# Kernel tuning notes

Hardware: AMD Instinct MI355X
Metric: run time of the kernel (lower is better)

The kernel has to match this reference:

```python
import jax, jax.numpy as jnp
import numpy as np

F_DIM = 1024
D = F_DIM // 2          # trunk width (divisor=2)
T = 1024                # contextlen
B = 32
PI = 256
VF = 256
N_HEADS = 4
EPS = 1e-5


def _posenc(seq_len, d):
    pos = jnp.arange(seq_len, dtype=jnp.float32)[:, None]
    div = jnp.exp(jnp.arange(0, d, 2, dtype=jnp.float32) * (-np.log(10000.0) / d))
    pe = jnp.zeros((seq_len, d), dtype=jnp.float32)
    pe = pe.at[:, 0::2].set(jnp.sin(pos * div))
    pe = pe.at[:, 1::2].set(jnp.cos(pos * div))
    return pe


def _ln(x, g, b):
    mu = x.mean(-1, keepdims=True)
    var = ((x - mu) ** 2).mean(-1, keepdims=True)
    return (x - mu) / jnp.sqrt(var + EPS) * g + b


def setup_inputs() -> dict:
    key = jax.random.key(0)
    ks = iter(jax.random.split(key, 40))
    w = lambda shape: jax.random.normal(next(ks), shape, dtype=jnp.float32) * 0.02
    inp = {
        "features": jax.random.normal(next(ks), (B, T, F_DIM), dtype=jnp.float32),
        "enc_w1": w((F_DIM, D)), "enc_b1": jnp.zeros((D,), jnp.float32),
        "enc_w2": w((D, D)),     "enc_b2": jnp.zeros((D,), jnp.float32),
        "qkv_w": w((D, 3 * D)),  "qkv_b": jnp.zeros((3 * D,), jnp.float32),
        "lam": jnp.float32(0.8),
        "out_w": w((D, D)),      "out_b": jnp.zeros((D,), jnp.float32),
        "ln1_g": jnp.ones((D,), jnp.float32), "ln1_b": jnp.zeros((D,), jnp.float32),
        "ffn_w1": w((D, F_DIM)), "ffn_b1": jnp.zeros((F_DIM,), jnp.float32),
        "ffn_w2": w((F_DIM, D)), "ffn_b2": jnp.zeros((D,), jnp.float32),
        "ln2_g": jnp.ones((D,), jnp.float32), "ln2_b": jnp.zeros((D,), jnp.float32),
        "act_w1": w((D, F_DIM)),       "act_b1": jnp.zeros((F_DIM,), jnp.float32),
        "act_w2": w((F_DIM, 2 * F_DIM)), "act_b2": jnp.zeros((2 * F_DIM,), jnp.float32),
        "act_w3": w((2 * F_DIM, PI)),  "act_b3": jnp.zeros((PI,), jnp.float32),
        "cr_w1": w((D, F_DIM)),        "cr_b1": jnp.zeros((F_DIM,), jnp.float32),
        "cr_w2": w((F_DIM, 2 * F_DIM)), "cr_b2": jnp.zeros((2 * F_DIM,), jnp.float32),
        "cr_w3": w((2 * F_DIM, VF)),   "cr_b3": jnp.zeros((VF,), jnp.float32),
    }
    return inp


def reference(features, enc_w1, enc_b1, enc_w2, enc_b2, qkv_w, qkv_b, lam,
              out_w, out_b, ln1_g, ln1_b, ffn_w1, ffn_b1, ffn_w2, ffn_b2,
              ln2_g, ln2_b, act_w1, act_b1, act_w2, act_b2, act_w3, act_b3,
              cr_w1, cr_b1, cr_w2, cr_b2, cr_w3, cr_b3):
    b, t, f = features.shape
    # encoder MLP: feature_dim -> d -> d with ReLU
    y = jax.nn.relu(features @ enc_w1 + enc_b1)
    y = jax.nn.relu(y @ enc_w2 + enc_b2)            # (B,T,D)
    d = y.shape[-1]
    y = y + _posenc(t, d)
    # differential dual-softmax attention (no head split; head_dim only scales)
    qkv = y @ qkv_w + qkv_b
    q, k, v = jnp.split(qkv, 3, axis=-1)
    q1, q2 = jnp.split(q, 2, axis=-1)
    k1, k2 = jnp.split(k, 2, axis=-1)
    scale = 1.0 / np.sqrt(d // N_HEADS)
    a1 = jax.nn.softmax(jnp.einsum('btc,bsc->bts', q1, k1) * scale, axis=-1)
    a2 = jax.nn.softmax(jnp.einsum('btc,bsc->bts', q2, k2) * scale, axis=-1)
    diff = a1 - lam * a2
    attn = jnp.einsum('bts,bsd->btd', diff, v)      # (B,T,D)
    # faithful to torch: transpose(0,1).contiguous().view(B,-1,D)
    attn = jnp.swapaxes(attn, 0, 1).reshape(b, t, d)
    attn = attn @ out_w + out_b
    y = _ln(y + attn, ln1_g, ln1_b)
    z = jax.nn.relu(y @ ffn_w1 + ffn_b1) @ ffn_w2 + ffn_b2
    y = _ln(y + z, ln2_g, ln2_b)                     # (B,T,D)
    # actor / critic heads, then take last timestep
    a = jax.nn.relu(y @ act_w1 + act_b1)
    a = jax.nn.relu(a @ act_w2 + act_b2)
    a = a @ act_w3 + act_b3
    c = jax.nn.relu(y @ cr_w1 + cr_b1)
    c = jax.nn.relu(c @ cr_w2 + cr_b2)
    c = c @ cr_w3 + cr_b3
    return (a[:, -1, :], c[:, -1, :])
```

## Files before the change

kernel.cpp:

```cpp
#include <hip/hip_runtime.h>
#include <hip/hip_bf16.h>
#include <math.h>

#define TDIM 1024
#define FDIM 1024
#define DDIM 512

typedef __attribute__((ext_vector_type(8))) short bf16x8;
typedef __attribute__((ext_vector_type(4))) float f32x4;

__device__ __forceinline__ float posenc_val(int t, int c) {
    int j = c >> 1;
    float dv = expf(-9.210340371976184f * (float)(2 * j) * (1.0f / 512.0f));
    float arg = (float)t * dv;
    return (c & 1) ? cosf(arg) : sinf(arg);
}

__device__ __forceinline__ ushort f2bf(float f) {
    __hip_bfloat16 h = __float2bfloat16(f);
    return *reinterpret_cast<ushort*>(&h);
}

__global__ __launch_bounds__(256)
void conv_bf16(const float* __restrict__ src, ushort* __restrict__ dst, int n4)
{
    int i = blockIdx.x * 256 + threadIdx.x;
    if (i < n4) {
        float4 v = ((const float4*)src)[i];
        ushort4 o;
        o.x = f2bf(v.x); o.y = f2bf(v.y); o.z = f2bf(v.z); o.w = f2bf(v.w);
        ((ushort4*)dst)[i] = o;
    }
}

__global__ __launch_bounds__(256)
void convT_bf16(const float* __restrict__ W, int ldw, int col0,
                ushort* __restrict__ Wt, int K)
{
    __shared__ float t[32][33];
    const int k0 = blockIdx.y * 32, n0 = blockIdx.x * 32;
    const int x = threadIdx.x & 31, y = threadIdx.x >> 5;
    #pragma unroll
    for (int yy = y; yy < 32; yy += 8)
        t[yy][x] = W[(size_t)(k0 + yy) * ldw + col0 + n0 + x];
    __syncthreads();
    #pragma unroll
    for (int yy = y; yy < 32; yy += 8)
        Wt[(size_t)(n0 + yy) * K + k0 + x] = f2bf(t[x][yy]);
}

__global__ __launch_bounds__(256)
void mfma_gemm(const ushort* __restrict__ A, const ushort* __restrict__ Bt,
               const float* __restrict__ bias,
               float* __restrict__ C, int ldc,
               ushort* __restrict__ Cbf, int ldcb,
               int K, int relu, int addpe)
{
    __shared__ __align__(16) ushort Al[64 * 64];
    __shared__ __align__(16) ushort Bl[64 * 64];
    const int tid = threadIdx.x;
    const int m0 = blockIdx.y * 64;
    const int n0 = blockIdx.x * 64;
    const int lane = tid & 63;
    const int wv = tid >> 6;
    const int wr = wv >> 1, wc = wv & 1;
    const int fr = lane & 15, g = lane >> 4;

    f32x4 acc[2][2] = {};

    const int r0 = tid >> 3;
    const int c0 = tid & 7;

    for (int k0 = 0; k0 < K; k0 += 64) {
        #pragma unroll
        for (int it = 0; it < 2; ++it) {
            int r = r0 + it * 32;
            uint4 va = *(const uint4*)(A + (size_t)(m0 + r) * K + k0 + c0 * 8);
            *(uint4*)((char*)Al + r * 128 + ((c0 ^ (r & 7)) << 4)) = va;
            uint4 vb = *(const uint4*)(Bt + (size_t)(n0 + r) * K + k0 + c0 * 8);
            *(uint4*)((char*)Bl + r * 128 + ((c0 ^ (r & 7)) << 4)) = vb;
        }
        __syncthreads();
        #pragma unroll
        for (int h = 0; h < 2; ++h) {
            bf16x8 af[2], bff[2];
            #pragma unroll
            for (int i = 0; i < 2; ++i) {
                int row = wr * 32 + i * 16 + fr;
                af[i] = *(const bf16x8*)((const char*)Al + row * 128 + (((h * 4 + g) ^ (row & 7)) << 4));
                int col = wc * 32 + i * 16 + fr;
                bff[i] = *(const bf16x8*)((const char*)Bl + col * 128 + (((h * 4 + g) ^ (col & 7)) << 4));
            }
            #pragma unroll
            for (int i = 0; i < 2; ++i)
                #pragma unroll
                for (int j = 0; j < 2; ++j)
                    acc[i][j] = __builtin_amdgcn_mfma_f32_16x16x32_bf16(af[i], bff[j], acc[i][j], 0, 0, 0);
        }
        __syncthreads();
    }

    #pragma unroll
    for (int j = 0; j < 2; ++j) {
        int n = n0 + wc * 32 + j * 16 + fr;
        float bv = bias ? bias[n] : 0.f;
        #pragma unroll
        for (int i = 0; i < 2; ++i) {
            #pragma unroll
            for (int q = 0; q < 4; ++q) {
                int m = m0 + wr * 32 + i * 16 + g * 4 + q;
                float v = acc[i][j][q] + bv;
                if (relu) v = fmaxf(v, 0.f);
                if (addpe) v += posenc_val(m, n);
                if (C)   C[(size_t)m * ldc + n] = v;
                if (Cbf) Cbf[(size_t)m * ldcb + n] = f2bf(v);
            }
        }
    }
}

template<int BK>
__global__ __launch_bounds__(256)
void gemm32d(const float* __restrict__ X0, const float* __restrict__ X1, long lda,
             const float* __restrict__ W0, const float* __restrict__ W1, long ldb,
             float* __restrict__ P, int N)
{
    __shared__ float Xs[32][BK + 4];
    __shared__ float Ws[BK][64];
    const float* A = blockIdx.z ? X1 : X0;
    const float* B = blockIdx.z ? W1 : W0;
    const int tid = threadIdx.x;
    const int n0 = blockIdx.x * 64;
    const int k0 = blockIdx.y * BK;

    {
        const int m  = tid >> 3;
        const int ks = (tid & 7) * (BK / 8);
        const float* src = A + (size_t)m * lda + k0 + ks;
        #pragma unroll
        for (int j = 0; j < BK / 32; ++j) {
            float4 v = *(const float4*)(src + j * 4);
            *(float4*)&Xs[m][ks + j * 4] = v;
        }
    }
    #pragma unroll
    for (int it = 0; it < BK / 16; ++it) {
        int e4  = it * 256 + tid;
        int row = e4 >> 4;
        int c4  = e4 & 15;
        float4 v = *(const float4*)(B + (size_t)(k0 + row) * ldb + n0 + c4 * 4);
        *(float4*)&Ws[row][c4 * 4] = v;
    }
    __syncthreads();

    const int tx = tid & 31;
    const int ty = tid >> 5;
    float acc[4][2] = {};
    #pragma unroll 8
    for (int k = 0; k < BK; k += 4) {
        float4 xv[4];
        #pragma unroll
        for (int i = 0; i < 4; ++i) xv[i] = *(const float4*)&Xs[ty * 4 + i][k];
        #pragma unroll
        for (int j = 0; j < 4; ++j) {
            float2 w = *(const float2*)&Ws[k + j][tx * 2];
            #pragma unroll
            for (int i = 0; i < 4; ++i) {
                float x = ((const float*)&xv[i])[j];
                acc[i][0] = fmaf(x, w.x, acc[i][0]);
                acc[i][1] = fmaf(x, w.y, acc[i][1]);
            }
        }
    }

    float* dst = P + (size_t)(blockIdx.z * gridDim.y + blockIdx.y) * 32 * N;
    #pragma unroll
    for (int i = 0; i < 4; ++i) {
        float2 v = make_float2(acc[i][0], acc[i][1]);
        *(float2*)(dst + (size_t)(ty * 4 + i) * N + n0 + tx * 2) = v;
    }
}

__global__ __launch_bounds__(256)
void finalized(const float* __restrict__ P, int KC, int N,
               const float* __restrict__ b0, const float* __restrict__ b1,
               float* __restrict__ Y0, float* __restrict__ Y1, int ldy,
               int do_relu, int perow)
{
    const int z = blockIdx.z;
    const float* bias = z ? b1 : b0;
    float* Y = z ? Y1 : Y0;
    const float* Pz = P + (size_t)z * KC * 32 * N;
    const int n = blockIdx.x * 256 + threadIdx.x;
    const int m = blockIdx.y;
    float s = bias ? bias[n] : 0.f;
    for (int kc = 0; kc < KC; ++kc) s += Pz[(size_t)(kc * 32 + m) * N + n];
    if (do_relu) s = fmaxf(s, 0.f);
    if (perow >= 0) s += posenc_val(perow, n);
    Y[(size_t)m * ldy + n] = s;
}

__global__ __launch_bounds__(256)
void scores_kernel(const float* __restrict__ KV, const float* __restrict__ Q32,
                   float* __restrict__ Psc)
{
    __shared__ float Kt[64][132];
    __shared__ float Qt[32][133];
    const int tid = threadIdx.x;
    const int s0 = blockIdx.x * 64;
    const int k0 = blockIdx.y * 128;

    #pragma unroll
    for (int it = 0; it < 8; ++it) {
        int e4 = it * 256 + tid;
        int r  = e4 >> 5;
        int c4 = e4 & 31;
        float4 v = *(const float4*)(KV + (size_t)(s0 + r) * 1024 + k0 + c4 * 4);
        *(float4*)&Kt[r][c4 * 4] = v;
    }
    #pragma unroll
    for (int it = 0; it < 4; ++it) {
        int e4 = it * 256 + tid;
        int r  = e4 >> 5;
        int c4 = e4 & 31;
        float4 v = *(const float4*)(Q32 + (size_t)r * 512 + k0 + c4 * 4);
        Qt[r][c4 * 4 + 0] = v.x;
        Qt[r][c4 * 4 + 1] = v.y;
        Qt[r][c4 * 4 + 2] = v.z;
        Qt[r][c4 * 4 + 3] = v.w;
    }
    __syncthreads();

    const int i  = tid & 31;
    const int sg = tid >> 5;
    float acc[8] = {};
    for (int k = 0; k < 128; ++k) {
        float q = Qt[i][k];
        #pragma unroll
        for (int j = 0; j < 8; ++j)
            acc[j] = fmaf(Kt[sg * 8 + j][k], q, acc[j]);
    }
    float* dst = Psc + (size_t)blockIdx.y * 1024 * 32;
    #pragma unroll
    for (int j = 0; j < 8; ++j)
        dst[(size_t)(s0 + sg * 8 + j) * 32 + i] = acc[j];
}

__global__ __launch_bounds__(256)
void softmax_diff(const float* __restrict__ Psc, const float* __restrict__ lam_p,
                  float* __restrict__ D)
{
    __shared__ float sc1[TDIM];
    __shared__ float sc2[TDIM];
    __shared__ float red[256];
    const int i = blockIdx.x;
    const int tid = threadIdx.x;
    const float scale = 0.08838834764831845f;
    for (int s = tid; s < TDIM; s += 256) {
        float a = Psc[(size_t)(0 * 1024 + s) * 32 + i] + Psc[(size_t)(1 * 1024 + s) * 32 + i];
        float b = Psc[(size_t)(2 * 1024 + s) * 32 + i] + Psc[(size_t)(3 * 1024 + s) * 32 + i];
        sc1[s] = a * scale;
        sc2[s] = b * scale;
    }
    __syncthreads();
    float m1 = -INFINITY, m2 = -INFINITY;
    for (int s = tid; s < TDIM; s += 256) { m1 = fmaxf(m1, sc1[s]); m2 = fmaxf(m2, sc2[s]); }
    red[tid] = m1; __syncthreads();
    for (int o = 128; o > 0; o >>= 1) { if (tid < o) red[tid] = fmaxf(red[tid], red[tid + o]); __syncthreads(); }
    m1 = red[0]; __syncthreads();
    red[tid] = m2; __syncthreads();
    for (int o = 128; o > 0; o >>= 1) { if (tid < o) red[tid] = fmaxf(red[tid], red[tid + o]); __syncthreads(); }
    m2 = red[0]; __syncthreads();
    float t1 = 0.f, t2 = 0.f;
    for (int s = tid; s < TDIM; s += 256) { t1 += expf(sc1[s] - m1); t2 += expf(sc2[s] - m2); }
    red[tid] = t1; __syncthreads();
    for (int o = 128; o > 0; o >>= 1) { if (tid < o) red[tid] += red[tid + o]; __syncthreads(); }
    t1 = red[0]; __syncthreads();
    red[tid] = t2; __syncthreads();
    for (int o = 128; o > 0; o >>= 1) { if (tid < o) red[tid] += red[tid + o]; __syncthreads(); }
    t2 = red[0]; __syncthreads();
    const float inv1 = 1.f / t1, inv2 = 1.f / t2;
    const float lam = *lam_p;
    for (int s = tid; s < TDIM; s += 256)
        D[(size_t)i * TDIM + s] = expf(sc1[s] - m1) * inv1 - lam * expf(sc2[s] - m2) * inv2;
}

__global__ __launch_bounds__(256)
void ln_kernel(const float* __restrict__ X, const float* __restrict__ R,
               const float* __restrict__ g, const float* __restrict__ b,
               float* __restrict__ Y)
{
    __shared__ float red[256];
    const int m = blockIdx.x;
    const int tid = threadIdx.x;
    float v0 = X[m * DDIM + tid]       + R[m * DDIM + tid];
    float v1 = X[m * DDIM + 256 + tid] + R[m * DDIM + 256 + tid];
    red[tid] = v0 + v1; __syncthreads();
    for (int o = 128; o > 0; o >>= 1) { if (tid < o) red[tid] += red[tid + o]; __syncthreads(); }
    const float mu = red[0] * (1.0f / 512.0f);
    __syncthreads();
    float d0 = v0 - mu, d1 = v1 - mu;
    red[tid] = d0 * d0 + d1 * d1; __syncthreads();
    for (int o = 128; o > 0; o >>= 1) { if (tid < o) red[tid] += red[tid + o]; __syncthreads(); }
    const float var = red[0] * (1.0f / 512.0f);
    const float inv = 1.0f / sqrtf(var + 1e-5f);
    Y[m * DDIM + tid]       = d0 * inv * g[tid]       + b[tid];
    Y[m * DDIM + 256 + tid] = d1 * inv * g[256 + tid] + b[256 + tid];
}

static void smallM2(const float* A0, const float* A1, long lda,
                    const float* B0, const float* B1, long ldb,
                    const float* b0, const float* b1,
                    float* Y0, float* Y1, int ldy, int K, int N,
                    int relu, int perow, float* P, int nz, hipStream_t stream)
{
    const int BK = (K == 1024 && N == 2048) ? 128 : 64;
    const int KC = K / BK;
    dim3 blk(256);
    if (BK == 128)
        gemm32d<128><<<dim3(N / 64, KC, nz), blk, 0, stream>>>(A0, A1, lda, B0, B1, ldb, P, N);
    else
        gemm32d<64><<<dim3(N / 64, KC, nz), blk, 0, stream>>>(A0, A1, lda, B0, B1, ldb, P, N);
    finalized<<<dim3(N / 256, 32, nz), blk, 0, stream>>>(P, KC, N, b0, b1, Y0, Y1, ldy, relu, perow);
}

extern "C" void kernel_launch(void* const* d_in, const int* in_sizes, int n_in,
                              void* d_out, int out_size, void* d_ws, size_t ws_size,
                              hipStream_t stream)
{
    const float* features = (const float*)d_in[0];
    const float* enc_w1 = (const float*)d_in[1];
    const float* enc_b1 = (const float*)d_in[2];
    const float* enc_w2 = (const float*)d_in[3];
    const float* enc_b2 = (const float*)d_in[4];
    const float* qkv_w  = (const float*)d_in[5];
    const float* qkv_b  = (const float*)d_in[6];
    const float* lam    = (const float*)d_in[7];
    const float* out_w  = (const float*)d_in[8];
    const float* out_b  = (const float*)d_in[9];
    const float* ln1_g  = (const float*)d_in[10];
    const float* ln1_b  = (const float*)d_in[11];
    const float* ffn_w1 = (const float*)d_in[12];
    const float* ffn_b1 = (const float*)d_in[13];
    const float* ffn_w2 = (const float*)d_in[14];
    const float* ffn_b2 = (const float*)d_in[15];
    const float* ln2_g  = (const float*)d_in[16];
    const float* ln2_b  = (const float*)d_in[17];
    const float* act_w1 = (const float*)d_in[18];
    const float* act_b1 = (const float*)d_in[19];
    const float* act_w2 = (const float*)d_in[20];
    const float* act_b2 = (const float*)d_in[21];
    const float* act_w3 = (const float*)d_in[22];
    const float* act_b3 = (const float*)d_in[23];
    const float* cr_w1  = (const float*)d_in[24];
    const float* cr_b1  = (const float*)d_in[25];
    const float* cr_w2  = (const float*)d_in[26];
    const float* cr_b2  = (const float*)d_in[27];
    const float* cr_w3  = (const float*)d_in[28];
    const float* cr_b3  = (const float*)d_in[29];
    float* out = (float*)d_out;

    char* base = (char*)d_ws;
    ushort* feat_bf = (ushort*)(base + 0);
    ushort* w1T     = (ushort*)(base + (2u << 20));
    ushort* w2T     = (ushort*)(base + (3u << 20));
    ushort* kvwT    = (ushort*)(base + 3670016);
    float*  Ppart   = (float*)(base + 0);
    ushort* H1bf    = (ushort*)(base + 4718592);
    float*  Y31     = (float*)(base + 5767168);
    ushort* Y31bf   = (ushort*)(base + 7864320);
    float*  KV      = (float*)(base + 8912896);
    float*  Psc     = (float*)(base + 13107200);
    float*  Dbuf    = (float*)(base + 13631488);
    float*  h32     = (float*)(base + 13762560);
    float*  ylast   = h32    + 32 * 512;
    float*  Q32     = ylast  + 32 * 512;
    float*  attn32  = Q32    + 32 * 512;
    float*  attnp   = attn32 + 32 * 512;
    float*  y1      = attnp  + 32 * 512;
    float*  y2      = y1     + 32 * 512;
    float*  zbuf    = y2     + 32 * 512;
    float*  hbufA   = zbuf   + 32 * 512;
    float*  hbufC   = hbufA  + 32 * 1024;
    float*  hbuf2A  = hbufC  + 32 * 1024;
    float*  hbuf2C  = hbuf2A + 32 * 2048;

    dim3 blk(256);

    conv_bf16<<<1024, blk, 0, stream>>>(features + (size_t)31 * TDIM * FDIM, feat_bf, 262144);
    convT_bf16<<<dim3(16, 32), blk, 0, stream>>>(enc_w1, DDIM, 0, w1T, FDIM);
    convT_bf16<<<dim3(16, 16), blk, 0, stream>>>(enc_w2, DDIM, 0, w2T, DDIM);
    convT_bf16<<<dim3(32, 16), blk, 0, stream>>>(qkv_w, 1536, 512, kvwT, DDIM);

    mfma_gemm<<<dim3(8, 16), blk, 0, stream>>>(feat_bf, w1T, enc_b1,
                                               (float*)nullptr, 0, H1bf, DDIM, FDIM, 1, 0);
    mfma_gemm<<<dim3(8, 16), blk, 0, stream>>>(H1bf, w2T, enc_b2,
                                               Y31, DDIM, Y31bf, DDIM, DDIM, 1, 1);
    mfma_gemm<<<dim3(16, 16), blk, 0, stream>>>(Y31bf, kvwT, qkv_b + 512,
                                                KV, 1024, (ushort*)nullptr, 0, DDIM, 0, 0);

    smallM2(features + (size_t)(TDIM - 1) * FDIM, nullptr, (long)TDIM * FDIM,
            enc_w1, nullptr, DDIM, enc_b1, nullptr, h32, nullptr, DDIM,
            FDIM, DDIM, 1, -1, Ppart, 1, stream);
    smallM2(h32, nullptr, DDIM, enc_w2, nullptr, DDIM, enc_b2, nullptr,
            ylast, nullptr, DDIM, DDIM, DDIM, 1, TDIM - 1, Ppart, 1, stream);
    smallM2(Y31 + 31 * DDIM, nullptr, 32 * DDIM, qkv_w, nullptr, 1536, qkv_b, nullptr,
            Q32, nullptr, DDIM, DDIM, DDIM, 0, -1, Ppart, 1, stream);

    scores_kernel<<<dim3(16, 4), blk, 0, stream>>>(KV, Q32, Psc);
    softmax_diff<<<32, blk, 0, stream>>>(Psc, lam, Dbuf);
    gemm32d<64><<<dim3(8, 16, 1), blk, 0, stream>>>(Dbuf, nullptr, 1024, KV + 512, nullptr, 1024, Ppart, 512);
    finalized<<<dim3(2, 32, 1), blk, 0, stream>>>(Ppart, 16, 512, nullptr, nullptr, attn32, nullptr, 512, 0, -1);

    smallM2(attn32, nullptr, DDIM, out_w, nullptr, DDIM, out_b, nullptr,
            attnp, nullptr, DDIM, DDIM, DDIM, 0, -1, Ppart, 1, stream);
    ln_kernel<<<32, blk, 0, stream>>>(ylast, attnp, ln1_g, ln1_b, y1);
    smallM2(y1, nullptr, DDIM, ffn_w1, nullptr, FDIM, ffn_b1, nullptr,
            hbufA, nullptr, FDIM, DDIM, FDIM, 1, -1, Ppart, 1, stream);
    smallM2(hbufA, nullptr, FDIM, ffn_w2, nullptr, DDIM, ffn_b2, nullptr,
            zbuf, nullptr, DDIM, FDIM, DDIM, 0, -1, Ppart, 1, stream);
    ln_kernel<<<32, blk, 0, stream>>>(y1, zbuf, ln2_g, ln2_b, y2);

    smallM2(y2, y2, DDIM, act_w1, cr_w1, FDIM, act_b1, cr_b1,
            hbufA, hbufC, FDIM, DDIM, FDIM, 1, -1, Ppart, 2, stream);
    smallM2(hbufA, hbufC, FDIM, act_w2, cr_w2, 2 * FDIM, act_b2, cr_b2,
            hbuf2A, hbuf2C, 2 * FDIM, FDIM, 2 * FDIM, 1, -1, Ppart, 2, stream);
    smallM2(hbuf2A, hbuf2C, 2 * FDIM, act_w3, cr_w3, 256, act_b3, cr_b3,
            out, out + 8192, 256, 2 * FDIM, 256, 0, -1, Ppart, 2, stream);
}
```

Measured before the change: 175.6 us.

## Fuse small kernels, merge split-K reductions into consumers, cut launch count

Merges the weight transposes and the first last-row GEMM into one prep kernel, and fuses the fp32-to-bf16 feature conversion into the MFMA GEMM's A load. Several independent stages are co-scheduled in shared launches. Split-K finalize kernels are removed by having the next GEMM or LayerNorm sum the partial buffers with bias and relu on load. The full QKV projection is computed in one MFMA GEMM, so the separate Q GEMM goes away. This cuts launch count and intermediate round trips, at the cost of redundant partial-sum reads inside each consumer block.

```diff
diff --git a/kernel.cpp b/kernel.cpp
--- a/kernel.cpp
+++ b/kernel.cpp
@@ -7,6 +7,7 @@
 #define DDIM 512
 
 typedef __attribute__((ext_vector_type(8))) short bf16x8;
+typedef __attribute__((ext_vector_type(8))) ushort u16x8;
 typedef __attribute__((ext_vector_type(4))) float f32x4;
 
 __device__ __forceinline__ float posenc_val(int t, int c) {
@@ -21,24 +22,102 @@
     return *reinterpret_cast<ushort*>(&h);
 }
 
-__global__ __launch_bounds__(256)
-void conv_bf16(const float* __restrict__ src, ushort* __restrict__ dst, int n4)
-{
-    int i = blockIdx.x * 256 + threadIdx.x;
-    if (i < n4) {
-        float4 v = ((const float4*)src)[i];
-        ushort4 o;
-        o.x = f2bf(v.x); o.y = f2bf(v.y); o.z = f2bf(v.z); o.w = f2bf(v.w);
-        ((ushort4*)dst)[i] = o;
-    }
-}
-
-__global__ __launch_bounds__(256)
-void convT_bf16(const float* __restrict__ W, int ldw, int col0,
-                ushort* __restrict__ Wt, int K)
-{
-    __shared__ float t[32][33];
-    const int k0 = blockIdx.y * 32, n0 = blockIdx.x * 32;
+template<int BK>
+__device__ __forceinline__ void g32_body(
+    const float* X, long lda,
+    const float* Pin, int KCx, const float* xbias, int xrelu,
+    const float* W, long ldb,
+    float* Pout, int N, int K,
+    int bx, int by, float* lds)
+{
+    float (*Xs)[BK + 4] = (float (*)[BK + 4])lds;
+    float (*Ws)[64]     = (float (*)[64])(lds + 32 * (BK + 4));
+    const int tid = threadIdx.x;
+    const int n0 = bx * 64, k0 = by * BK;
+
+    {
+        const int m  = tid >> 3;
+        const int ks = (tid & 7) * (BK / 8);
+        if (Pin) {
+            #pragma unroll
+            for (int j = 0; j < BK / 32; ++j) {
+                float4 a = make_float4(0.f, 0.f, 0.f, 0.f);
+                for (int c = 0; c < KCx; ++c) {
+                    float4 v = *(const float4*)(Pin + (size_t)(c * 32 + m) * K + k0 + ks + j * 4);
+                    a.x += v.x; a.y += v.y; a.z += v.z; a.w += v.w;
+                }
+                if (xbias) {
+                    float4 bv = *(const float4*)(xbias + k0 + ks + j * 4);
+                    a.x += bv.x; a.y += bv.y; a.z += bv.z; a.w += bv.w;
+                }
+                if (xrelu) {
+                    a.x = fmaxf(a.x, 0.f); a.y = fmaxf(a.y, 0.f);
+                    a.z = fmaxf(a.z, 0.f); a.w = fmaxf(a.w, 0.f);
+                }
+                *(float4*)&Xs[m][ks + j * 4] = a;
+            }
+        } else {
+            const float* src = X + (size_t)m * lda + k0 + ks;
+            #pragma unroll
+            for (int j = 0; j < BK / 32; ++j)
+                *(float4*)&Xs[m][ks + j * 4] = *(const float4*)(src + j * 4);
+        }
+    }
+    #pragma unroll
+    for (int it = 0; it < BK / 16; ++it) {
+        int e4  = it * 256 + tid;
+        int row = e4 >> 4;
+        int c4  = e4 & 15;
+        *(float4*)&Ws[row][c4 * 4] = *(const float4*)(W + (size_t)(k0 + row) * ldb + n0 + c4 * 4);
+    }
+    __syncthreads();
+
+    const int tx = tid & 31;
+    const int ty = tid >> 5;
+    float acc[4][2] = {};
+    #pragma unroll 8
+    for (int k = 0; k < BK; k += 4) {
+        float4 xv[4];
+        #pragma unroll
+        for (int i = 0; i < 4; ++i) xv[i] = *(const float4*)&Xs[ty * 4 + i][k];
+        #pragma unroll
+        for (int j = 0; j < 4; ++j) {
+            float2 w = *(const float2*)&Ws[k + j][tx * 2];
+            #pragma unroll
+            for (int i = 0; i < 4; ++i) {
+                float x = ((const float*)&xv[i])[j];
+                acc[i][0] = fmaf(x, w.x, acc[i][0]);
+                acc[i][1] = fmaf(x, w.y, acc[i][1]);
+            }
+        }
+    }
+    float* dst = Pout + (size_t)by * 32 * N;
+    #pragma unroll
+    for (int i = 0; i < 4; ++i)
+        *(float2*)(dst + (size_t)(ty * 4 + i) * N + n0 + tx * 2) = make_float2(acc[i][0], acc[i][1]);
+}
+
+template<int BK>
+__global__ __launch_bounds__(256) void g32k(
+    const float* X0, const float* X1, long lda,
+    const float* Pin0, const float* Pin1, int KCx,
+    const float* xb0, const float* xb1, int xrelu,
+    const float* W0, const float* W1, long ldb,
+    float* Pout, int N, int K)
+{
+    __shared__ __align__(16) float lds[32 * (BK + 4) + BK * 64];
+    const int z = blockIdx.z;
+    g32_body<BK>(z ? X1 : X0, lda, z ? Pin1 : Pin0, KCx, z ? xb1 : xb0, xrelu,
+                 z ? W1 : W0, ldb,
+                 Pout + (size_t)z * gridDim.y * 32 * N,
+                 N, K, blockIdx.x, blockIdx.y, lds);
+}
+
+__device__ __forceinline__ void convT_body(const float* W, int ldw, int col0,
+                                           ushort* Wt, int K, int bx, int by, float* lds)
+{
+    float (*t)[33] = (float (*)[33])lds;
+    const int k0 = by * 32, n0 = bx * 32;
     const int x = threadIdx.x & 31, y = threadIdx.x >> 5;
     #pragma unroll
     for (int yy = y; yy < 32; yy += 8)
@@ -49,18 +128,18 @@
         Wt[(size_t)(n0 + yy) * K + k0 + x] = f2bf(t[x][yy]);
 }
 
-__global__ __launch_bounds__(256)
-void mfma_gemm(const ushort* __restrict__ A, const ushort* __restrict__ Bt,
-               const float* __restrict__ bias,
-               float* __restrict__ C, int ldc,
-               ushort* __restrict__ Cbf, int ldcb,
-               int K, int relu, int addpe)
-{
-    __shared__ __align__(16) ushort Al[64 * 64];
-    __shared__ __align__(16) ushort Bl[64 * 64];
+__device__ __forceinline__ void mfma_body(
+    const void* Aptr, int af32, long lda,
+    const ushort* Bt, const float* bias,
+    float* C, int ldc, ushort* Cbf, int ldcb,
+    int K, int relu, int addpe,
+    int bx, int by, char* smem)
+{
+    ushort* Al = (ushort*)smem;
+    ushort* Bl = Al + 64 * 64;
     const int tid = threadIdx.x;
-    const int m0 = blockIdx.y * 64;
-    const int n0 = blockIdx.x * 64;
+    const int m0 = by * 64;
+    const int n0 = bx * 64;
     const int lane = tid & 63;
     const int wv = tid >> 6;
     const int wr = wv >> 1, wc = wv & 1;
@@ -75,8 +154,20 @@
         #pragma unroll
         for (int it = 0; it < 2; ++it) {
             int r = r0 + it * 32;
-            uint4 va = *(const uint4*)(A + (size_t)(m0 + r) * K + k0 + c0 * 8);
-            *(uint4*)((char*)Al + r * 128 + ((c0 ^ (r & 7)) << 4)) = va;
+            if (af32) {
+                const float* Af = (const float*)Aptr;
+                const float* s = Af + (size_t)(m0 + r) * lda + k0 + c0 * 8;
+                float4 u = *(const float4*)s;
+                float4 v = *(const float4*)(s + 4);
+                u16x8 pv;
+                pv[0] = f2bf(u.x); pv[1] = f2bf(u.y); pv[2] = f2bf(u.z); pv[3] = f2bf(u.w);
+                pv[4] = f2bf(v.x); pv[5] = f2bf(v.y); pv[6] = f2bf(v.z); pv[7] = f2bf(v.w);
+                *(u16x8*)((char*)Al + r * 128 + ((c0 ^ (r & 7)) << 4)) = pv;
+            } else {
+                const ushort* Au = (const ushort*)Aptr;
+                uint4 va = *(const uint4*)(Au + (size_t)(m0 + r) * lda + k0 + c0 * 8);
+                *(uint4*)((char*)Al + r * 128 + ((c0 ^ (r & 7)) << 4)) = va;
+            }
             uint4 vb = *(const uint4*)(Bt + (size_t)(n0 + r) * K + k0 + c0 * 8);
             *(uint4*)((char*)Bl + r * 128 + ((c0 ^ (r & 7)) << 4)) = vb;
         }
@@ -119,103 +210,67 @@
     }
 }
 
-template<int BK>
-__global__ __launch_bounds__(256)
-void gemm32d(const float* __restrict__ X0, const float* __restrict__ X1, long lda,
-             const float* __restrict__ W0, const float* __restrict__ W1, long ldb,
-             float* __restrict__ P, int N)
-{
-    __shared__ float Xs[32][BK + 4];
-    __shared__ float Ws[BK][64];
-    const float* A = blockIdx.z ? X1 : X0;
-    const float* B = blockIdx.z ? W1 : W0;
+__global__ __launch_bounds__(256) void mfma_k(
+    const void* A, int af32, long lda, const ushort* Bt, const float* bias,
+    float* C, int ldc, ushort* Cbf, int ldcb, int K, int relu, int pe)
+{
+    __shared__ __align__(16) char smem[16384];
+    mfma_body(A, af32, lda, Bt, bias, C, ldc, Cbf, ldcb, K, relu, pe,
+              blockIdx.x, blockIdx.y, smem);
+}
+
+__global__ __launch_bounds__(256) void prep_k(
+    const float* features, const float* enc_w1, const float* qkv_w, const float* enc_w2,
+    ushort* w1T, ushort* w2T, ushort* qkvT, float* P_enc1)
+{
+    __shared__ __align__(16) float lds[6272];
+    int t = blockIdx.x;
+    if (t < 128) {
+        g32_body<64>(features + (size_t)1023 * FDIM, (long)TDIM * FDIM,
+                     nullptr, 0, nullptr, 0,
+                     enc_w1, DDIM, P_enc1, 512, 1024, t & 7, t >> 3, lds);
+    } else if (t < 640) {
+        int u = t - 128;
+        convT_body(enc_w1, 512, 0, w1T, 1024, u & 15, u >> 4, lds);
+    } else if (t < 896) {
+        int u = t - 640;
+        convT_body(enc_w2, 512, 0, w2T, 512, u & 15, u >> 4, lds);
+    } else {
+        int u = t - 896;
+        convT_body(qkv_w, 1536, 0, qkvT, 512, u % 48, u / 48, lds);
+    }
+}
+
+__global__ __launch_bounds__(256) void stage2_k(
+    const float* features31, const ushort* w1T, const float* enc_b1, ushort* H1bf,
+    const float* P_enc1, const float* enc_w2, float* P_enc2)
+{
+    __shared__ __align__(16) char smem[25600];
+    int t = blockIdx.x;
+    if (t < 128) {
+        mfma_body(features31, 1, 1024, w1T, enc_b1, nullptr, 0, H1bf, 512,
+                  1024, 1, 0, t & 7, t >> 3, smem);
+    } else {
+        int u = t - 128;
+        g32_body<64>(nullptr, 0, P_enc1, 16, enc_b1, 1,
+                     enc_w2, 512, P_enc2, 512, 512, u & 7, u >> 3, (float*)smem);
+    }
+}
+
+__device__ void scores_body(const float* QKV, float* Psc, int bxs, int byc, char* smem)
+{
+    float (*Kt)[132] = (float (*)[132])smem;
+    float (*Qt)[133] = (float (*)[133])(smem + 64 * 132 * 4);
     const int tid = threadIdx.x;
-    const int n0 = blockIdx.x * 64;
-    const int k0 = blockIdx.y * BK;
-
-    {
-        const int m  = tid >> 3;
-        const int ks = (tid & 7) * (BK / 8);
-        const float* src = A + (size_t)m * lda + k0 + ks;
-        #pragma unroll
-        for (int j = 0; j < BK / 32; ++j) {
-            float4 v = *(const float4*)(src + j * 4);
-            *(float4*)&Xs[m][ks + j * 4] = v;
-        }
-    }
-    #pragma unroll
-    for (int it = 0; it < BK / 16; ++it) {
-        int e4  = it * 256 + tid;
-        int row = e4 >> 4;
-        int c4  = e4 & 15;
-        float4 v = *(const float4*)(B + (size_t)(k0 + row) * ldb + n0 + c4 * 4);
-        *(float4*)&Ws[row][c4 * 4] = v;
-    }
-    __syncthreads();
-
-    const int tx = tid & 31;
-    const int ty = tid >> 5;
-    float acc[4][2] = {};
-    #pragma unroll 8
-    for (int k = 0; k < BK; k += 4) {
-        float4 xv[4];
-        #pragma unroll
-        for (int i = 0; i < 4; ++i) xv[i] = *(const float4*)&Xs[ty * 4 + i][k];
-        #pragma unroll
-        for (int j = 0; j < 4; ++j) {
-            float2 w = *(const float2*)&Ws[k + j][tx * 2];
-            #pragma unroll
-            for (int i = 0; i < 4; ++i) {
-                float x = ((const float*)&xv[i])[j];
-                acc[i][0] = fmaf(x, w.x, acc[i][0]);
-                acc[i][1] = fmaf(x, w.y, acc[i][1]);
-            }
-        }
-    }
-
-    float* dst = P + (size_t)(blockIdx.z * gridDim.y + blockIdx.y) * 32 * N;
-    #pragma unroll
-    for (int i = 0; i < 4; ++i) {
-        float2 v = make_float2(acc[i][0], acc[i][1]);
-        *(float2*)(dst + (size_t)(ty * 4 + i) * N + n0 + tx * 2) = v;
-    }
-}
-
-__global__ __launch_bounds__(256)
-void finalized(const float* __restrict__ P, int KC, int N,
-               const float* __restrict__ b0, const float* __restrict__ b1,
-               float* __restrict__ Y0, float* __restrict__ Y1, int ldy,
-               int do_relu, int perow)
-{
-    const int z = blockIdx.z;
-    const float* bias = z ? b1 : b0;
-    float* Y = z ? Y1 : Y0;
-    const float* Pz = P + (size_t)z * KC * 32 * N;
-    const int n = blockIdx.x * 256 + threadIdx.x;
-    const int m = blockIdx.y;
-    float s = bias ? bias[n] : 0.f;
-    for (int kc = 0; kc < KC; ++kc) s += Pz[(size_t)(kc * 32 + m) * N + n];
-    if (do_relu) s = fmaxf(s, 0.f);
-    if (perow >= 0) s += posenc_val(perow, n);
-    Y[(size_t)m * ldy + n] = s;
-}
-
-__global__ __launch_bounds__(256)
-void scores_kernel(const float* __restrict__ KV, const float* __restrict__ Q32,
-                   float* __restrict__ Psc)
-{
-    __shared__ float Kt[64][132];
-    __shared__ float Qt[32][133];
-    const int tid = threadIdx.x;
-    const int s0 = blockIdx.x * 64;
-    const int k0 = blockIdx.y * 128;
+    const int s0 = bxs * 64;
+    const int k0 = byc * 128;
 
     #pragma unroll
     for (int it = 0; it < 8; ++it) {
         int e4 = it * 256 + tid;
         int r  = e4 >> 5;
         int c4 = e4 & 31;
-        float4 v = *(const float4*)(KV + (size_t)(s0 + r) * 1024 + k0 + c4 * 4);
+        float4 v = *(const float4*)(QKV + (size_t)(s0 + r) * 1536 + 512 + k0 + c4 * 4);
         *(float4*)&Kt[r][c4 * 4] = v;
     }
     #pragma unroll
@@ -223,7 +278,7 @@
         int e4 = it * 256 + tid;
         int r  = e4 >> 5;
         int c4 = e4 & 31;
-        float4 v = *(const float4*)(Q32 + (size_t)r * 512 + k0 + c4 * 4);
+        float4 v = *(const float4*)(QKV + (size_t)(32 * r + 31) * 1536 + k0 + c4 * 4);
         Qt[r][c4 * 4 + 0] = v.x;
         Qt[r][c4 * 4 + 1] = v.y;
         Qt[r][c4 * 4 + 2] = v.z;
@@ -240,15 +295,35 @@
         for (int j = 0; j < 8; ++j)
             acc[j] = fmaf(Kt[sg * 8 + j][k], q, acc[j]);
     }
-    float* dst = Psc + (size_t)blockIdx.y * 1024 * 32;
+    float* dst = Psc + (size_t)byc * 1024 * 32;
     #pragma unroll
     for (int j = 0; j < 8; ++j)
         dst[(size_t)(s0 + sg * 8 + j) * 32 + i] = acc[j];
 }
 
-__global__ __launch_bounds__(256)
-void softmax_diff(const float* __restrict__ Psc, const float* __restrict__ lam_p,
-                  float* __restrict__ D)
+__global__ __launch_bounds__(256) void stage5_k(
+    const float* QKV, float* Psc,
+    const float* P_enc2, const float* enc_b2, float* ylast)
+{
+    __shared__ __align__(16) char smem[50816];
+    int t = blockIdx.x;
+    if (t < 64) {
+        scores_body(QKV, Psc, t & 15, t >> 4, smem);
+    } else {
+        int blk = t - 64;
+        for (int idx = threadIdx.x; idx < 4 * 512; idx += 256) {
+            int r = idx >> 9, c = idx & 511;
+            int m = blk * 4 + r;
+            float s = enc_b2[c];
+            for (int cc = 0; cc < 8; ++cc) s += P_enc2[(size_t)(cc * 32 + m) * 512 + c];
+            s = fmaxf(s, 0.f) + posenc_val(1023, c);
+            ylast[m * 512 + c] = s;
+        }
+    }
+}
+
+__global__ __launch_bounds__(256) void softmax_diff(
+    const float* __restrict__ Psc, const float* __restrict__ lam_p, float* __restrict__ D)
 {
     __shared__ float sc1[TDIM];
     __shared__ float sc2[TDIM];
@@ -285,16 +360,22 @@
         D[(size_t)i * TDIM + s] = expf(sc1[s] - m1) * inv1 - lam * expf(sc2[s] - m2) * inv2;
 }
 
-__global__ __launch_bounds__(256)
-void ln_kernel(const float* __restrict__ X, const float* __restrict__ R,
-               const float* __restrict__ g, const float* __restrict__ b,
-               float* __restrict__ Y)
+__global__ __launch_bounds__(256) void ln_red(
+    const float* __restrict__ Pin, int KC, const float* __restrict__ bias,
+    const float* __restrict__ R, const float* __restrict__ g, const float* __restrict__ b,
+    float* __restrict__ Y)
 {
     __shared__ float red[256];
     const int m = blockIdx.x;
     const int tid = threadIdx.x;
-    float v0 = X[m * DDIM + tid]       + R[m * DDIM + tid];
-    float v1 = X[m * DDIM + 256 + tid] + R[m * DDIM + 256 + tid];
+    float v0 = bias ? bias[tid] : 0.f;
+    float v1 = bias ? bias[tid + 256] : 0.f;
+    for (int c = 0; c < KC; ++c) {
+        v0 += Pin[(size_t)(c * 32 + m) * 512 + tid];
+        v1 += Pin[(size_t)(c * 32 + m) * 512 + tid + 256];
+    }
+    v0 += R[m * 512 + tid];
+    v1 += R[m * 512 + tid + 256];
     red[tid] = v0 + v1; __syncthreads();
     for (int o = 128; o > 0; o >>= 1) { if (tid < o) red[tid] += red[tid + o]; __syncthreads(); }
     const float mu = red[0] * (1.0f / 512.0f);
@@ -304,24 +385,22 @@
     for (int o = 128; o > 0; o >>= 1) { if (tid < o) red[tid] += red[tid + o]; __syncthreads(); }
     const float var = red[0] * (1.0f / 512.0f);
     const float inv = 1.0f / sqrtf(var + 1e-5f);
-    Y[m * DDIM + tid]       = d0 * inv * g[tid]       + b[tid];
-    Y[m * DDIM + 256 + tid] = d1 * inv * g[256 + tid] + b[256 + tid];
-}
-
-static void smallM2(const float* A0, const float* A1, long lda,
-                    const float* B0, const float* B1, long ldb,
-                    const float* b0, const float* b1,
-                    float* Y0, float* Y1, int ldy, int K, int N,
-                    int relu, int perow, float* P, int nz, hipStream_t stream)
-{
-    const int BK = (K == 1024 && N == 2048) ? 128 : 64;
-    const int KC = K / BK;
-    dim3 blk(256);
-    if (BK == 128)
-        gemm32d<128><<<dim3(N / 64, KC, nz), blk, 0, stream>>>(A0, A1, lda, B0, B1, ldb, P, N);
-    else
-        gemm32d<64><<<dim3(N / 64, KC, nz), blk, 0, stream>>>(A0, A1, lda, B0, B1, ldb, P, N);
-    finalized<<<dim3(N / 256, 32, nz), blk, 0, stream>>>(P, KC, N, b0, b1, Y0, Y1, ldy, relu, perow);
+    Y[m * 512 + tid]       = d0 * inv * g[tid]       + b[tid];
+    Y[m * 512 + 256 + tid] = d1 * inv * g[256 + tid] + b[256 + tid];
+}
+
+__global__ __launch_bounds__(256) void fin_out(
+    const float* __restrict__ P, const float* __restrict__ b0, const float* __restrict__ b1,
+    float* __restrict__ out)
+{
+    const int m = blockIdx.x;
+    const int z = blockIdx.y;
+    const int n = threadIdx.x;
+    const float* bias = z ? b1 : b0;
+    const float* Pz = P + (size_t)z * 16 * 32 * 256;
+    float s = bias[n];
+    for (int c = 0; c < 16; ++c) s += Pz[(size_t)(c * 32 + m) * 256 + n];
+    out[z * 8192 + m * 256 + n] = s;
 }
 
 extern "C" void kernel_launch(void* const* d_in, const int* in_sizes, int n_in,
@@ -361,70 +440,56 @@
     float* out = (float*)d_out;
 
     char* base = (char*)d_ws;
-    ushort* feat_bf = (ushort*)(base + 0);
-    ushort* w1T     = (ushort*)(base + (2u << 20));
-    ushort* w2T     = (ushort*)(base + (3u << 20));
-    ushort* kvwT    = (ushort*)(base + 3670016);
-    float*  Ppart   = (float*)(base + 0);
-    ushort* H1bf    = (ushort*)(base + 4718592);
-    float*  Y31     = (float*)(base + 5767168);
-    ushort* Y31bf   = (ushort*)(base + 7864320);
-    float*  KV      = (float*)(base + 8912896);
-    float*  Psc     = (float*)(base + 13107200);
-    float*  Dbuf    = (float*)(base + 13631488);
-    float*  h32     = (float*)(base + 13762560);
-    float*  ylast   = h32    + 32 * 512;
-    float*  Q32     = ylast  + 32 * 512;
-    float*  attn32  = Q32    + 32 * 512;
-    float*  attnp   = attn32 + 32 * 512;
-    float*  y1      = attnp  + 32 * 512;
-    float*  y2      = y1     + 32 * 512;
-    float*  zbuf    = y2     + 32 * 512;
-    float*  hbufA   = zbuf   + 32 * 512;
-    float*  hbufC   = hbufA  + 32 * 1024;
-    float*  hbuf2A  = hbufC  + 32 * 1024;
-    float*  hbuf2C  = hbuf2A + 32 * 2048;
-
+    ushort* w1T    = (ushort*)(base + 0x000000);
+    ushort* w2T    = (ushort*)(base + 0x100000);
+    ushort* qkvT   = (ushort*)(base + 0x180000);
+    ushort* H1bf   = (ushort*)(base + 0x300000);
+    ushort* Y31bf  = (ushort*)(base + 0x400000);
+    float*  QKV    = (float*)(base + 0x500000);
+    float*  Psc    = (float*)(base + 0xB00000);
+    float*  Dbuf   = (float*)(base + 0xB80000);
+    float*  ylast  = (float*)(base + 0xBA0000);
+    float*  y1     = (float*)(base + 0xBB0000);
+    float*  y2     = (float*)(base + 0xBC0000);
+    float*  P_enc1 = (float*)(base + 0xC00000);
+    float*  P_enc2 = (float*)(base + 0xD00000);
+    float*  P_attn = (float*)(base + 0xD80000);
+    float*  P_atp  = (float*)(base + 0xE80000);
+    float*  P_h    = (float*)(base + 0xF00000);
+    float*  P_z    = (float*)(base + 0x1000000);
+    float*  P_a1   = (float*)(base + 0x1100000);
+    float*  P_a2   = (float*)(base + 0x1300000);
+    float*  P_a3   = (float*)(base + 0x1700000);
+
+    const float* features31 = features + (size_t)31 * TDIM * FDIM;
     dim3 blk(256);
-
-    conv_bf16<<<1024, blk, 0, stream>>>(features + (size_t)31 * TDIM * FDIM, feat_bf, 262144);
-    convT_bf16<<<dim3(16, 32), blk, 0, stream>>>(enc_w1, DDIM, 0, w1T, FDIM);
-    convT_bf16<<<dim3(16, 16), blk, 0, stream>>>(enc_w2, DDIM, 0, w2T, DDIM);
-    convT_bf16<<<dim3(32, 16), blk, 0, stream>>>(qkv_w, 1536, 512, kvwT, DDIM);
-
-    mfma_gemm<<<dim3(8, 16), blk, 0, stream>>>(feat_bf, w1T, enc_b1,
-                                               (float*)nullptr, 0, H1bf, DDIM, FDIM, 1, 0);
-    mfma_gemm<<<dim3(8, 16), blk, 0, stream>>>(H1bf, w2T, enc_b2,
-                                               Y31, DDIM, Y31bf, DDIM, DDIM, 1, 1);
-    mfma_gemm<<<dim3(16, 16), blk, 0, stream>>>(Y31bf, kvwT, qkv_b + 512,
-                                                KV, 1024, (ushort*)nullptr, 0, DDIM, 0, 0);
-
-    smallM2(features + (size_t)(TDIM - 1) * FDIM, nullptr, (long)TDIM * FDIM,
-            enc_w1, nullptr, DDIM, enc_b1, nullptr, h32, nullptr, DDIM,
-            FDIM, DDIM, 1, -1, Ppart, 1, stream);
-    smallM2(h32, nullptr, DDIM, enc_w2, nullptr, DDIM, enc_b2, nullptr,
-            ylast, nullptr, DDIM, DDIM, DDIM, 1, TDIM - 1, Ppart, 1, stream);
-    smallM2(Y31 + 31 * DDIM, nullptr, 32 * DDIM, qkv_w, nullptr, 1536, qkv_b, nullptr,
-            Q32, nullptr, DDIM, DDIM, DDIM, 0, -1, Ppart, 1, stream);
-
-    scores_kernel<<<dim3(16, 4), blk, 0, stream>>>(KV, Q32, Psc);
+    const float* NPF = nullptr;
+
+    prep_k<<<1664, blk, 0, stream>>>(features, enc_w1, qkv_w, enc_w2, w1T, w2T, qkvT, P_enc1);
+    stage2_k<<<192, blk, 0, stream>>>(features31, w1T, enc_b1, H1bf, P_enc1, enc_w2, P_enc2);
+    mfma_k<<<dim3(8, 16), blk, 0, stream>>>(H1bf, 0, 512, w2T, enc_b2,
+                                            nullptr, 0, Y31bf, 512, 512, 1, 1);
+    mfma_k<<<dim3(24, 16), blk, 0, stream>>>(Y31bf, 0, 512, qkvT, qkv_b,
+                                             QKV, 1536, nullptr, 0, 512, 0, 0);
+    stage5_k<<<72, blk, 0, stream>>>(QKV, Psc, P_enc2, enc_b2, ylast);
     softmax_diff<<<32, blk, 0, stream>>>(Psc, lam, Dbuf);
-    gemm32d<64><<<dim3(8, 16, 1), blk, 0, stream>>>(Dbuf, nullptr, 1024, KV + 512, nullptr, 1024, Ppart, 512);
-    finalized<<<dim3(2, 32, 1), blk, 0, stream>>>(Ppart, 16, 512, nullptr, nullptr, attn32, nullptr, 512, 0, -1);
-
-    smallM2(attn32, nullptr, DDIM, out_w, nullptr, DDIM, out_b, nullptr,
-            attnp, nullptr, DDIM, DDIM, DDIM, 0, -1, Ppart, 1, stream);
-    ln_kernel<<<32, blk, 0, stream>>>(ylast, attnp, ln1_g, ln1_b, y1);
-    smallM2(y1, nullptr, DDIM, ffn_w1, nullptr, FDIM, ffn_b1, nullptr,
-            hbufA, nullptr, FDIM, DDIM, FDIM, 1, -1, Ppart, 1, stream);
-    smallM2(hbufA, nullptr, FDIM, ffn_w2, nullptr, DDIM, ffn_b2, nullptr,
-            zbuf, nullptr, DDIM, FDIM, DDIM, 0, -1, Ppart, 1, stream);
-    ln_kernel<<<32, blk, 0, stream>>>(y1, zbuf, ln2_g, ln2_b, y2);
-
-    smallM2(y2, y2, DDIM, act_w1, cr_w1, FDIM, act_b1, cr_b1,
-            hbufA, hbufC, FDIM, DDIM, FDIM, 1, -1, Ppart, 2, stream);
-    smallM2(hbufA, hbufC, FDIM, act_w2, cr_w2, 2 * FDIM, act_b2, cr_b2,
-            hbuf2A, hbuf2C, 2 * FDIM, FDIM, 2 * FDIM, 1, -1, Ppart, 2, stream);
-    smallM2(hbuf2A, hbuf2C, 2 * FDIM, act_w3, cr_w3, 256, act_b3, cr_b3,
-            out, out + 8192, 256, 2 * FDIM, 256, 0, -1, Ppart, 2, stream);
-}
+    g32k<64><<<dim3(8, 16, 1), blk, 0, stream>>>(Dbuf, NPF, 1024, NPF, NPF, 0, NPF, NPF, 0,
+                                                 QKV + 1024, NPF, 1536, P_attn, 512, 1024);
+    g32k<64><<<dim3(8, 8, 1), blk, 0, stream>>>(NPF, NPF, 0, P_attn, NPF, 16, NPF, NPF, 0,
+                                                out_w, NPF, 512, P_atp, 512, 512);
+    ln_red<<<32, blk, 0, stream>>>(P_atp, 8, out_b, ylast, ln1_g, ln1_b, y1);
+    g32k<64><<<dim3(16, 8, 1), blk, 0, stream>>>(y1, NPF, 512, NPF, NPF, 0, NPF, NPF, 0,
+                                                 ffn_w1, NPF, 1024, P_h, 1024, 512);
+    g32k<64><<<dim3(8, 16, 1), blk, 0, stream>>>(NPF, NPF, 0, P_h, NPF, 8, ffn_b1, NPF, 1,
+                                                 ffn_w2, NPF, 512, P_z, 512, 1024);
+    ln_red<<<32, blk, 0, stream>>>(P_z, 16, ffn_b2, y1, ln2_g, ln2_b, y2);
+    g32k<64><<<dim3(16, 8, 2), blk, 0, stream>>>(y2, y2, 512, NPF, NPF, 0, NPF, NPF, 0,
+                                                 act_w1, cr_w1, 1024, P_a1, 1024, 512);
+    g32k<128><<<dim3(32, 8, 2), blk, 0, stream>>>(NPF, NPF, 0, P_a1, P_a1 + 8 * 32 * 1024, 8,
+                                                  act_b1, cr_b1, 1,
+                                                  act_w2, cr_w2, 2048, P_a2, 2048, 1024);
+    g32k<128><<<dim3(4, 16, 2), blk, 0, stream>>>(NPF, NPF, 0, P_a2, P_a2 + 8 * 32 * 2048, 8,
+                                                  act_b2, cr_b2, 1,
+                                                  act_w3, cr_w3, 256, P_a3, 256, 2048);
+    fin_out<<<dim3(32, 2), blk, 0, stream>>>(P_a3, act_b3, cr_b3, out);
+}
```

Measured after the change: 141.6 us. 1.24x faster.
